# Performance work log

Measured on AMD Instinct MI355X. Metric: run time of the kernel, lower is better.

## Reference

```python
import jax, jax.numpy as jnp
import numpy as np
from jax import lax

PADLEN = 9  # 3 * max(len(a), len(b)) for an order-2 filter (3 taps each)


def _butter2_lowpass(cutoff, fs):
    # 2nd-order Butterworth lowpass via bilinear transform; matches
    # scipy.signal.butter(2, 2*cutoff/fs, btype='lowpass', output='ba')
    c = 1.0 / np.tan(np.pi * cutoff / fs)
    a0 = 1.0 + np.sqrt(2.0) * c + c * c
    b = np.array([1.0, 2.0, 1.0]) / a0
    a = np.array([a0, 2.0 - 2.0 * c * c, 1.0 - np.sqrt(2.0) * c + c * c]) / a0
    return b.astype(np.float32), a.astype(np.float32)


def setup_inputs() -> dict:
    key = jax.random.key(0)
    x = jax.random.normal(key, (16, 64, 48000), dtype=jnp.float32)
    b, a = _butter2_lowpass(1000.0, 48000.0)
    return {"x": x, "b": jnp.asarray(b), "a": jnp.asarray(a)}


def _pad_odd(x, n):
    # Odd-reflection padding, identical to _BaseFilter._pad_odd
    left_end = x[..., 0:1]
    left_ext = jnp.flip(x[..., 0:n], axis=-1)
    right_end = x[..., -1:]
    right_ext = jnp.flip(x[..., -(n + 2):-2], axis=-1)
    return jnp.concatenate((2.0 * left_end - left_ext, x, 2.0 * right_end - right_ext), axis=-1)


def _lfilter(x, a, b):
    # x: (N, T). Direct-form II transposed IIR with zero initial conditions
    # (same semantics as torchaudio.functional.lfilter, clamp=False).
    a0 = a[0]
    a_n = a / a0
    b_n = b / a0
    order = a.shape[0] - 1
    b0 = b_n[0]
    b_rest = b_n[1:]  # (order,)
    a_rest = a_n[1:]  # (order,)

    def step(z, xt):
        # z: (N, order) filter state, xt: (N,)
        y = b0 * xt + z[:, 0]
        z_new = xt[:, None] * b_rest - y[:, None] * a_rest
        z_new = z_new.at[:, :-1].add(z[:, 1:])
        return z_new, y

    z0 = jnp.zeros((x.shape[0], order), x.dtype)
    _, y = lax.scan(step, z0, x.T)  # y: (T, N)
    return y.T


def _filtfilt(x, a, b):
    # torchaudio.functional.filtfilt: forward lfilter (clamp=False), then
    # reversed lfilter with clamp=True (default), then reverse.
    fwd = _lfilter(x, a, b)
    bwd = _lfilter(jnp.flip(fwd, axis=-1), a, b)
    return jnp.clip(jnp.flip(bwd, axis=-1), -1.0, 1.0)


def reference(x, b, a):
    shape = x.shape
    scale = jnp.max(jnp.abs(x), axis=-1, keepdims=True)
    xn = x / scale
    xp = _pad_odd(xn, PADLEN)                     # (..., T + 2*PADLEN)
    x2 = xp.reshape(-1, xp.shape[-1])             # flatten lanes for the scan
    y2 = _filtfilt(x2, a, b)
    y = y2.reshape(shape[:-1] + (y2.shape[-1],))
    y = y[..., PADLEN:-PADLEN]                    # unpad back to T
    return y * scale
```

## Files before the change

### kernel.cpp

```cpp
#include <hip/hip_runtime.h>

#define NROWS 1024
#define N     48000
#define PAD   9
#define NPADE (N + PAD)

#define CL  32
#define W   2048
#define WU  96
#define MW  1856
#define NB  26
#define WPB 4
#define NBLK (NROWS * NB / WPB)

#define SWZ(g) (((g) & ~7) | (((g) & 7) ^ (((g) >> 3) & 7)))

__device__ __forceinline__ float rfl(float v) {
    return __int_as_float(__builtin_amdgcn_readfirstlane(__float_as_int(v)));
}

__device__ __forceinline__ float xt_fetch(const float* __restrict__ xr, int t) {
    if (t < -PAD || t >= NPADE) return 0.0f;
    if (t < 0)  return 2.0f * xr[0]     - xr[-1 - t];
    if (t < N)  return xr[t];
    return 2.0f * xr[N - 1] - xr[2 * N - 3 - t];
}

#define FS(px,py,pz,pw,d) { float l0 = __shfl_up(s0, d), l1 = __shfl_up(s1, d);   \
    if (lane >= d) { s0 = fmaf(px, l0, fmaf(py, l1, s0));                         \
                     s1 = fmaf(pz, l0, fmaf(pw, l1, s1)); } }
#define BS(px,py,pz,pw,d) { float l0 = __shfl_down(s0, d), l1 = __shfl_down(s1, d);\
    if (lane < 64 - d) { s0 = fmaf(px, l0, fmaf(py, l1, s0));                     \
                         s1 = fmaf(pz, l0, fmaf(pw, l1, s1)); } }

#define SQR() { float t00 = m00*m00 + m01*m10, t01 = m00*m01 + m01*m11;           \
                float t10 = m10*m00 + m11*m10, t11 = m10*m01 + m11*m11;           \
                m00 = t00; m01 = t01; m10 = t10; m11 = t11; }

__global__ __launch_bounds__(256, 4) void filt_kernel(
    const float* __restrict__ x,
    const float* __restrict__ bc,
    const float* __restrict__ ac,
    float* __restrict__ out)
{
    __shared__ float lds[WPB * W];

    const int lane = threadIdx.x & 63;
    const int wid  = threadIdx.x >> 6;
    const unsigned w  = blockIdx.x * WPB + wid;
    const unsigned r  = w / (unsigned)NB;
    const unsigned wb = w - r * (unsigned)NB;
    const int tb0 = (int)wb * MW - WU;
    const int tb  = tb0 + lane * CL;

    const float b0  = rfl(bc[0]), b1 = rfl(bc[1]), b2 = rfl(bc[2]);
    const float na1 = rfl(-ac[1]), na2 = rfl(-ac[2]);
    const float* xr = x + (size_t)r * N;
    float* orow = out + (size_t)r * N;
    float* wbuf = lds + wid * W;

    float m00 = na1, m01 = 1.f, m10 = na2, m11 = 0.f;
    SQR() SQR() SQR() SQR() SQR()
    const float p0x=rfl(m00), p0y=rfl(m01), p0z=rfl(m10), p0w=rfl(m11); SQR()
    const float p1x=rfl(m00), p1y=rfl(m01), p1z=rfl(m10), p1w=rfl(m11); SQR()
    const float p2x=rfl(m00), p2y=rfl(m01), p2z=rfl(m10), p2w=rfl(m11);

    if (tb0 >= 0 && tb0 + W <= N) {
        const float4* src = (const float4*)(xr + tb0);
        #pragma unroll
        for (int m = 0; m < 8; ++m) {
            int g = m * 64 + lane;
            *(float4*)(wbuf + 4 * SWZ(g)) = src[g];
        }
    } else {
        #pragma unroll
        for (int m = 0; m < 8; ++m) {
            int g = m * 64 + lane;
            int t = tb0 + 4 * g;
            *(float4*)(wbuf + 4 * SWZ(g)) =
                make_float4(xt_fetch(xr, t),     xt_fetch(xr, t + 1),
                            xt_fetch(xr, t + 2), xt_fetch(xr, t + 3));
        }
    }
    float c[CL];
    #pragma unroll
    for (int k = 0; k < 8; ++k) {
        float4 v = *(const float4*)(wbuf + 4 * (8 * lane + (k ^ (lane & 7))));
        int kk = 4 * k;
        c[kk] = v.x; c[kk+1] = v.y; c[kk+2] = v.z; c[kk+3] = v.w;
    }

    float xm1 = 0.f, xm2 = 0.f, ym1 = 0.f, ym2 = 0.f;
    #pragma unroll
    for (int k = 0; k < CL; ++k) {
        float xk = c[k];
        float X  = fmaf(b1, xm1, b2 * xm2);
        X        = fmaf(b0, xk, X);
        float p  = fmaf(na2, ym2, X);
        float y  = fmaf(na1, ym1, p);
        c[k] = y;
        xm2 = xm1; xm1 = xk; ym2 = ym1; ym1 = y;
    }
    float s0 = fmaf(b1, xm1, b2 * xm2);
    s0 = fmaf(na1, ym1, s0); s0 = fmaf(na2, ym2, s0);
    float s1 = fmaf(na2, ym1, b2 * xm1);

    FS(p0x,p0y,p0z,p0w, 1) FS(p1x,p1y,p1z,p1w, 2) FS(p2x,p2y,p2z,p2w, 4)
    float in0 = __shfl_up(s0, 1), in1 = __shfl_up(s1, 1);
    if (lane == 0) { in0 = 0.f; in1 = 0.f; }

    {
        float hm = in0;
        float h  = fmaf(na1, in0, in1);
        c[0] += hm;
        #pragma unroll
        for (int k = 1; k < CL; ++k) {
            c[k] += h;
            float nh = fmaf(na1, h, na2 * hm);
            hm = h; h = nh;
        }
    }

    if (tb + CL > NPADE) {
        #pragma unroll
        for (int k = 0; k < CL; ++k)
            if (tb + k >= NPADE) c[k] = 0.f;
    }

    xm1 = 0.f; xm2 = 0.f; ym1 = 0.f; ym2 = 0.f;
    #pragma unroll
    for (int k = CL - 1; k >= 0; --k) {
        float xk = c[k];
        float X  = fmaf(b1, xm1, b2 * xm2);
        X        = fmaf(b0, xk, X);
        float p  = fmaf(na2, ym2, X);
        float y  = fmaf(na1, ym1, p);
        c[k] = y;
        xm2 = xm1; xm1 = xk; ym2 = ym1; ym1 = y;
    }
    s0 = fmaf(b1, xm1, b2 * xm2);
    s0 = fmaf(na1, ym1, s0); s0 = fmaf(na2, ym2, s0);
    s1 = fmaf(na2, ym1, b2 * xm1);

    BS(p0x,p0y,p0z,p0w, 1) BS(p1x,p1y,p1z,p1w, 2) BS(p2x,p2y,p2z,p2w, 4)
    in0 = __shfl_down(s0, 1); in1 = __shfl_down(s1, 1);
    if (lane == 63) { in0 = 0.f; in1 = 0.f; }

    {
        float hm = in0;
        float h  = fmaf(na1, in0, in1);
        c[CL - 1] += hm;
        #pragma unroll
        for (int k = CL - 2; k >= 0; --k) {
            c[k] += h;
            float nh = fmaf(na1, h, na2 * hm);
            hm = h; h = nh;
        }
    }

    #pragma unroll
    for (int k = 0; k < 8; ++k) {
        int kk = 4 * k;
        *(float4*)(wbuf + 4 * (8 * lane + (k ^ (lane & 7)))) =
            make_float4(c[kk], c[kk+1], c[kk+2], c[kk+3]);
    }
    #pragma unroll
    for (int m = 0; m < 8; ++m) {
        int g = m * 64 + lane;
        int t = tb0 + 4 * g;
        if (g >= WU / 4 && g < (WU + MW) / 4 && t + 4 <= N) {
            float4 v = *(const float4*)(wbuf + 4 * SWZ(g));
            *(float4*)(orow + t) = v;
        }
    }
}

extern "C" void kernel_launch(void* const* d_in, const int* in_sizes, int n_in,
                              void* d_out, int out_size, void* d_ws, size_t ws_size,
                              hipStream_t stream) {
    const float* x  = (const float*)d_in[0];
    const float* bc = (const float*)d_in[1];
    const float* ac = (const float*)d_in[2];
    float* out = (float*)d_out;

    filt_kernel<<<dim3(NBLK), dim3(256), 0, stream>>>(x, bc, ac, out);
}
```

Measured before the change: 79.91 us.

## Persistent waves with double-buffered async global-to-LDS prefetch of next window

The kernel becomes persistent: a fixed grid of 1280 blocks of 2 waves loops over all row windows. While the current window is computed, the next interior window is loaded straight into a second LDS buffer with global_load_lds, and an s_waitcnt vmcnt(8) waits only for the current buffer. Output stores switch to nontemporal. The aim is to hide global load latency behind the scan arithmetic. The risks are lower occupancy from fewer blocks, and the correctness of the vmcnt accounting, since boundary windows issue no prefetch and the LDS swizzle must match the global_load_lds lane mapping.

```diff
diff --git a/kernel.cpp b/kernel.cpp
--- a/kernel.cpp
+++ b/kernel.cpp
@@ -10,8 +10,12 @@
 #define WU  96
 #define MW  1856
 #define NB  26
-#define WPB 4
-#define NBLK (NROWS * NB / WPB)
+#define NWIN (NROWS * NB)
+#define WPB  2
+#define NBLK 1280
+#define NWAVES (NBLK * WPB)
+
+typedef float v4f __attribute__((ext_vector_type(4)));
 
 #define SWZ(g) (((g) & ~7) | (((g) & 7) ^ (((g) >> 3) & 7)))
 
@@ -37,27 +41,33 @@
                 float t10 = m10*m00 + m11*m10, t11 = m10*m01 + m11*m11;           \
                 m00 = t00; m01 = t01; m10 = t10; m11 = t11; }
 
-__global__ __launch_bounds__(256, 4) void filt_kernel(
+__device__ __forceinline__ void prefetch_win(const float* __restrict__ src,
+                                             int lane_swz,
+                                             float* __restrict__ slice) {
+    #pragma unroll
+    for (int m = 0; m < 8; ++m) {
+        __builtin_amdgcn_global_load_lds(
+            (const __attribute__((address_space(1))) float*)(src + 4 * (m * 64 + lane_swz)),
+            (__attribute__((address_space(3))) float*)(slice + 4 * (m * 64)),
+            16, 0, 0);
+    }
+}
+
+__global__ __launch_bounds__(128, 4) void filt_kernel(
     const float* __restrict__ x,
     const float* __restrict__ bc,
     const float* __restrict__ ac,
     float* __restrict__ out)
 {
-    __shared__ float lds[WPB * W];
+    __shared__ float lds[WPB][2][W];
 
     const int lane = threadIdx.x & 63;
     const int wid  = threadIdx.x >> 6;
-    const unsigned w  = blockIdx.x * WPB + wid;
-    const unsigned r  = w / (unsigned)NB;
-    const unsigned wb = w - r * (unsigned)NB;
-    const int tb0 = (int)wb * MW - WU;
-    const int tb  = tb0 + lane * CL;
+    const unsigned wave = blockIdx.x * WPB + wid;
+    const int lane_swz = (lane & ~7) | ((lane & 7) ^ ((lane >> 3) & 7));
 
     const float b0  = rfl(bc[0]), b1 = rfl(bc[1]), b2 = rfl(bc[2]);
     const float na1 = rfl(-ac[1]), na2 = rfl(-ac[2]);
-    const float* xr = x + (size_t)r * N;
-    float* orow = out + (size_t)r * N;
-    float* wbuf = lds + wid * W;
 
     float m00 = na1, m01 = 1.f, m10 = na2, m11 = 0.f;
     SQR() SQR() SQR() SQR() SQR()
@@ -65,113 +75,138 @@
     const float p1x=rfl(m00), p1y=rfl(m01), p1z=rfl(m10), p1w=rfl(m11); SQR()
     const float p2x=rfl(m00), p2y=rfl(m01), p2z=rfl(m10), p2w=rfl(m11);
 
-    if (tb0 >= 0 && tb0 + W <= N) {
-        const float4* src = (const float4*)(xr + tb0);
-        #pragma unroll
-        for (int m = 0; m < 8; ++m) {
-            int g = m * 64 + lane;
-            *(float4*)(wbuf + 4 * SWZ(g)) = src[g];
-        }
-    } else {
+    if (wave < NWIN) {
+        const unsigned r = wave / NB, wb = wave - r * NB;
+        const int tb0 = (int)wb * MW - WU;
+        if (tb0 >= 0 && tb0 + W <= N)
+            prefetch_win(x + (size_t)r * N + tb0, lane_swz, &lds[wid][0][0]);
+    }
+
+    int cur = 0;
+    for (unsigned i = wave; i < NWIN; i += NWAVES) {
+        const unsigned r  = i / NB, wb = i - r * NB;
+        const int tb0 = (int)wb * MW - WU;
+        const int tb  = tb0 + lane * CL;
+        const float* xr = x + (size_t)r * N;
+        float* orow = out + (size_t)r * N;
+        float* wbuf = &lds[wid][cur][0];
+        const bool interior = (tb0 >= 0) && (tb0 + W <= N);
+
+        const unsigned inx = i + NWAVES;
+        if (inx < NWIN) {
+            const unsigned rn = inx / NB, wbn = inx - rn * NB;
+            const int tb0n = (int)wbn * MW - WU;
+            if (tb0n >= 0 && tb0n + W <= N)
+                prefetch_win(x + (size_t)rn * N + tb0n, lane_swz,
+                             &lds[wid][cur ^ 1][0]);
+        }
+
+        asm volatile("s_waitcnt vmcnt(8)" ::: "memory");
+
+        if (!interior) {
+            #pragma unroll
+            for (int m = 0; m < 8; ++m) {
+                int g = m * 64 + lane;
+                int t = tb0 + 4 * g;
+                *(float4*)(wbuf + 4 * SWZ(g)) =
+                    make_float4(xt_fetch(xr, t),     xt_fetch(xr, t + 1),
+                                xt_fetch(xr, t + 2), xt_fetch(xr, t + 3));
+            }
+        }
+
+        float c[CL];
+        #pragma unroll
+        for (int k = 0; k < 8; ++k) {
+            float4 v = *(const float4*)(wbuf + 4 * (8 * lane + (k ^ (lane & 7))));
+            int kk = 4 * k;
+            c[kk] = v.x; c[kk+1] = v.y; c[kk+2] = v.z; c[kk+3] = v.w;
+        }
+
+        float xm1 = 0.f, xm2 = 0.f, ym1 = 0.f, ym2 = 0.f;
+        #pragma unroll
+        for (int k = 0; k < CL; ++k) {
+            float xk = c[k];
+            float X  = fmaf(b1, xm1, b2 * xm2);
+            X        = fmaf(b0, xk, X);
+            float p  = fmaf(na2, ym2, X);
+            float y  = fmaf(na1, ym1, p);
+            c[k] = y;
+            xm2 = xm1; xm1 = xk; ym2 = ym1; ym1 = y;
+        }
+        float s0 = fmaf(b1, xm1, b2 * xm2);
+        s0 = fmaf(na1, ym1, s0); s0 = fmaf(na2, ym2, s0);
+        float s1 = fmaf(na2, ym1, b2 * xm1);
+
+        FS(p0x,p0y,p0z,p0w, 1) FS(p1x,p1y,p1z,p1w, 2) FS(p2x,p2y,p2z,p2w, 4)
+        float in0 = __shfl_up(s0, 1), in1 = __shfl_up(s1, 1);
+        if (lane == 0) { in0 = 0.f; in1 = 0.f; }
+
+        {
+            float hm = in0;
+            float h  = fmaf(na1, in0, in1);
+            c[0] += hm;
+            #pragma unroll
+            for (int k = 1; k < CL; ++k) {
+                c[k] += h;
+                float nh = fmaf(na1, h, na2 * hm);
+                hm = h; h = nh;
+            }
+        }
+
+        if (tb + CL > NPADE) {
+            #pragma unroll
+            for (int k = 0; k < CL; ++k)
+                if (tb + k >= NPADE) c[k] = 0.f;
+        }
+
+        xm1 = 0.f; xm2 = 0.f; ym1 = 0.f; ym2 = 0.f;
+        #pragma unroll
+        for (int k = CL - 1; k >= 0; --k) {
+            float xk = c[k];
+            float X  = fmaf(b1, xm1, b2 * xm2);
+            X        = fmaf(b0, xk, X);
+            float p  = fmaf(na2, ym2, X);
+            float y  = fmaf(na1, ym1, p);
+            c[k] = y;
+            xm2 = xm1; xm1 = xk; ym2 = ym1; ym1 = y;
+        }
+        s0 = fmaf(b1, xm1, b2 * xm2);
+        s0 = fmaf(na1, ym1, s0); s0 = fmaf(na2, ym2, s0);
+        s1 = fmaf(na2, ym1, b2 * xm1);
+
+        BS(p0x,p0y,p0z,p0w, 1) BS(p1x,p1y,p1z,p1w, 2) BS(p2x,p2y,p2z,p2w, 4)
+        in0 = __shfl_down(s0, 1); in1 = __shfl_down(s1, 1);
+        if (lane == 63) { in0 = 0.f; in1 = 0.f; }
+
+        {
+            float hm = in0;
+            float h  = fmaf(na1, in0, in1);
+            c[CL - 1] += hm;
+            #pragma unroll
+            for (int k = CL - 2; k >= 0; --k) {
+                c[k] += h;
+                float nh = fmaf(na1, h, na2 * hm);
+                hm = h; h = nh;
+            }
+        }
+
+        #pragma unroll
+        for (int k = 0; k < 8; ++k) {
+            int kk = 4 * k;
+            *(float4*)(wbuf + 4 * (8 * lane + (k ^ (lane & 7)))) =
+                make_float4(c[kk], c[kk+1], c[kk+2], c[kk+3]);
+        }
         #pragma unroll
         for (int m = 0; m < 8; ++m) {
             int g = m * 64 + lane;
             int t = tb0 + 4 * g;
-            *(float4*)(wbuf + 4 * SWZ(g)) =
-                make_float4(xt_fetch(xr, t),     xt_fetch(xr, t + 1),
-                            xt_fetch(xr, t + 2), xt_fetch(xr, t + 3));
-        }
-    }
-    float c[CL];
-    #pragma unroll
-    for (int k = 0; k < 8; ++k) {
-        float4 v = *(const float4*)(wbuf + 4 * (8 * lane + (k ^ (lane & 7))));
-        int kk = 4 * k;
-        c[kk] = v.x; c[kk+1] = v.y; c[kk+2] = v.z; c[kk+3] = v.w;
-    }
-
-    float xm1 = 0.f, xm2 = 0.f, ym1 = 0.f, ym2 = 0.f;
-    #pragma unroll
-    for (int k = 0; k < CL; ++k) {
-        float xk = c[k];
-        float X  = fmaf(b1, xm1, b2 * xm2);
-        X        = fmaf(b0, xk, X);
-        float p  = fmaf(na2, ym2, X);
-        float y  = fmaf(na1, ym1, p);
-        c[k] = y;
-        xm2 = xm1; xm1 = xk; ym2 = ym1; ym1 = y;
-    }
-    float s0 = fmaf(b1, xm1, b2 * xm2);
-    s0 = fmaf(na1, ym1, s0); s0 = fmaf(na2, ym2, s0);
-    float s1 = fmaf(na2, ym1, b2 * xm1);
-
-    FS(p0x,p0y,p0z,p0w, 1) FS(p1x,p1y,p1z,p1w, 2) FS(p2x,p2y,p2z,p2w, 4)
-    float in0 = __shfl_up(s0, 1), in1 = __shfl_up(s1, 1);
-    if (lane == 0) { in0 = 0.f; in1 = 0.f; }
-
-    {
-        float hm = in0;
-        float h  = fmaf(na1, in0, in1);
-        c[0] += hm;
-        #pragma unroll
-        for (int k = 1; k < CL; ++k) {
-            c[k] += h;
-            float nh = fmaf(na1, h, na2 * hm);
-            hm = h; h = nh;
-        }
-    }
-
-    if (tb + CL > NPADE) {
-        #pragma unroll
-        for (int k = 0; k < CL; ++k)
-            if (tb + k >= NPADE) c[k] = 0.f;
-    }
-
-    xm1 = 0.f; xm2 = 0.f; ym1 = 0.f; ym2 = 0.f;
-    #pragma unroll
-    for (int k = CL - 1; k >= 0; --k) {
-        float xk = c[k];
-        float X  = fmaf(b1, xm1, b2 * xm2);
-        X        = fmaf(b0, xk, X);
-        float p  = fmaf(na2, ym2, X);
-        float y  = fmaf(na1, ym1, p);
-        c[k] = y;
-        xm2 = xm1; xm1 = xk; ym2 = ym1; ym1 = y;
-    }
-    s0 = fmaf(b1, xm1, b2 * xm2);
-    s0 = fmaf(na1, ym1, s0); s0 = fmaf(na2, ym2, s0);
-    s1 = fmaf(na2, ym1, b2 * xm1);
-
-    BS(p0x,p0y,p0z,p0w, 1) BS(p1x,p1y,p1z,p1w, 2) BS(p2x,p2y,p2z,p2w, 4)
-    in0 = __shfl_down(s0, 1); in1 = __shfl_down(s1, 1);
-    if (lane == 63) { in0 = 0.f; in1 = 0.f; }
-
-    {
-        float hm = in0;
-        float h  = fmaf(na1, in0, in1);
-        c[CL - 1] += hm;
-        #pragma unroll
-        for (int k = CL - 2; k >= 0; --k) {
-            c[k] += h;
-            float nh = fmaf(na1, h, na2 * hm);
-            hm = h; h = nh;
-        }
-    }
-
-    #pragma unroll
-    for (int k = 0; k < 8; ++k) {
-        int kk = 4 * k;
-        *(float4*)(wbuf + 4 * (8 * lane + (k ^ (lane & 7)))) =
-            make_float4(c[kk], c[kk+1], c[kk+2], c[kk+3]);
-    }
-    #pragma unroll
-    for (int m = 0; m < 8; ++m) {
-        int g = m * 64 + lane;
-        int t = tb0 + 4 * g;
-        if (g >= WU / 4 && g < (WU + MW) / 4 && t + 4 <= N) {
-            float4 v = *(const float4*)(wbuf + 4 * SWZ(g));
-            *(float4*)(orow + t) = v;
-        }
+            if (g >= WU / 4 && g < (WU + MW) / 4 && t + 4 <= N) {
+                v4f v = *(const v4f*)(wbuf + 4 * SWZ(g));
+                __builtin_nontemporal_store(v, (v4f*)(orow + t));
+            }
+        }
+
+        cur ^= 1;
     }
 }
 
@@ -183,5 +218,5 @@
     const float* ac = (const float*)d_in[2];
     float* out = (float*)d_out;
 
-    filt_kernel<<<dim3(NBLK), dim3(256), 0, stream>>>(x, bc, ac, out);
-}
+    filt_kernel<<<dim3(NBLK), dim3(128), 0, stream>>>(x, bc, ac, out);
+}
```

After: 86.85 us. +8.7%, slower.
